# Kernel optimization log

Hardware: AMD Instinct MI355X
Metric: run time of the kernel (lower is better)

## Reference

```python
import jax, jax.numpy as jnp
import numpy as np

TAU = 0.28
EPS = 1e-08

def _l2norm(x):
    # F.normalize(dim=1): x / max(||x||, 1e-12)
    n = jnp.sqrt(jnp.sum(x * x, axis=1, keepdims=True))
    return x / jnp.maximum(n, 1e-12)

def setup_inputs() -> dict:
    key = jax.random.key(0)
    k1, k2 = jax.random.split(key)
    N, D = 16384, 64
    return {
        "user_embed": jax.random.normal(k1, (N, D), dtype=jnp.float32),
        "pos_item_embed": jax.random.normal(k2, (N, D), dtype=jnp.float32),
    }

def reference(user_embed, pos_item_embed):
    u = _l2norm(user_embed)          # [N, D]
    i = _l2norm(pos_item_embed)      # [N, D]
    pos_score = jnp.exp(jnp.sum(u * i, axis=-1) / TAU)          # [N]
    ui = jnp.matmul(u, i.T)          # [N, N]
    uu = jnp.matmul(u, u.T)          # [N, N]
    total = jnp.sum(jnp.exp((ui + uu) / TAU), axis=1)           # [N]
    na_loss = -jnp.log(pos_score / (total + EPS))
    return jnp.mean(na_loss)
```

## Files before the change

kernel.cpp:

```cpp
#include <hip/hip_runtime.h>
#include <hip/hip_bf16.h>

#define NROWS 16384
#define DIM 64
#define BCOLS 512
#define BROWS 1024
#define NCS (NROWS / BCOLS)
#define NRG (NROWS / BROWS)

static constexpr float TAU = 0.28f;
static constexpr float EPS = 1e-8f;
static constexpr float EXP2_SCALE = (float)(1.0 / (0.28 * 0.6931471805599453));
static constexpr float LN2F = 0.69314718055994530942f;

using short8 = __attribute__((ext_vector_type(8))) short;
using f32x4  = __attribute__((ext_vector_type(4))) float;

typedef __attribute__((address_space(1))) const unsigned char ga_t;
typedef __attribute__((address_space(3))) unsigned char la_t;

__global__ __launch_bounds__(256) void prep_kernel(
    const float* __restrict__ u, const float* __restrict__ v,
    __hip_bfloat16* __restrict__ a_out, __hip_bfloat16* __restrict__ w_out,
    float* __restrict__ p_out, float* __restrict__ total, float* __restrict__ out)
{
    const int lane = threadIdx.x & 63;
    const int wv   = threadIdx.x >> 6;
    const int row  = blockIdx.x * 4 + wv;

    const float uu = u[row * DIM + lane];
    const float ii = v[row * DIM + lane];
    float su = uu * uu, si = ii * ii, sd = uu * ii;
#pragma unroll
    for (int m = 1; m < 64; m <<= 1) {
        su += __shfl_xor(su, m, 64);
        si += __shfl_xor(si, m, 64);
        sd += __shfl_xor(sd, m, 64);
    }
    const float inv_u = 1.0f / fmaxf(sqrtf(su), 1e-12f);
    const float inv_i = 1.0f / fmaxf(sqrtf(si), 1e-12f);
    const float un = uu * inv_u;
    const float in = ii * inv_i;
    a_out[row * DIM + lane] = __float2bfloat16(EXP2_SCALE * un);
    w_out[row * DIM + lane] = __float2bfloat16(un + in);
    if (lane == 0) {
        p_out[row] = sd * inv_u * inv_i * (1.0f / TAU);
        total[row] = 0.0f;
    }
    if (blockIdx.x == 0 && threadIdx.x == 0) out[0] = 0.0f;
}

__global__ __launch_bounds__(512, 4) void score_kernel(
    const __hip_bfloat16* __restrict__ A, const __hip_bfloat16* __restrict__ W,
    float* __restrict__ total)
{
    __shared__ alignas(16) ushort blds[BCOLS * DIM];

    const int tid  = threadIdx.x;
    const int lane = tid & 63;
    const int wv   = tid >> 6;
    const int l15  = lane & 15;
    const int quad = lane >> 4;
    const int cs   = blockIdx.x & (NCS - 1);
    const int rg   = blockIdx.x >> 5;
    const int col0    = cs * BCOLS;
    const int rowbase = rg * BROWS;

    const ushort* Au = (const ushort*)A;
    const ushort* Wu = (const ushort*)W;

#pragma unroll
    for (int q = 0; q < 8; q++) {
        const int p = q * 512 + tid;
        const int j = p >> 3;
        const int c = (p & 7) ^ (j & 7);
        const ushort* g = Wu + (size_t)(col0 + j) * DIM + c * 8;
        __builtin_amdgcn_global_load_lds((ga_t*)g, (la_t*)&blds[(size_t)p * 8], 16, 0, 0);
    }
    __syncthreads();

    for (int si = 0; si < 4; si++) {
        const int r0 = rowbase + wv * 128 + si * 32;

        short8 af[2][2];
#pragma unroll
        for (int rs = 0; rs < 2; rs++)
#pragma unroll
            for (int kk = 0; kk < 2; kk++)
                af[rs][kk] = *(const short8*)(
                    Au + (size_t)(r0 + rs * 16 + l15) * DIM + kk * 32 + quad * 8);

        float rowsum[2][4];
#pragma unroll
        for (int rs = 0; rs < 2; rs++)
#pragma unroll
            for (int r = 0; r < 4; r++) rowsum[rs][r] = 0.0f;

#pragma unroll 8
        for (int ct = 0; ct < BCOLS / 16; ct++) {
            const int jl = ct * 16 + l15;
            const int sw = l15 & 7;
            const short8 b0 = *(const short8*)&blds[(size_t)(jl * 8 + (quad ^ sw)) * 8];
            const short8 b1 = *(const short8*)&blds[(size_t)(jl * 8 + ((4 + quad) ^ sw)) * 8];
#pragma unroll
            for (int rs = 0; rs < 2; rs++) {
                f32x4 acc = {0.f, 0.f, 0.f, 0.f};
                acc = __builtin_amdgcn_mfma_f32_16x16x32_bf16(af[rs][0], b0, acc, 0, 0, 0);
                acc = __builtin_amdgcn_mfma_f32_16x16x32_bf16(af[rs][1], b1, acc, 0, 0, 0);
#pragma unroll
                for (int r = 0; r < 4; r++)
                    rowsum[rs][r] += __builtin_amdgcn_exp2f(acc[r]);
            }
        }

#pragma unroll
        for (int m = 1; m < 16; m <<= 1)
#pragma unroll
            for (int rs = 0; rs < 2; rs++)
#pragma unroll
                for (int r = 0; r < 4; r++)
                    rowsum[rs][r] += __shfl_xor(rowsum[rs][r], m, 64);

        if (l15 == 0) {
#pragma unroll
            for (int rs = 0; rs < 2; rs++)
#pragma unroll
                for (int r = 0; r < 4; r++)
                    atomicAdd(&total[r0 + rs * 16 + quad * 4 + r], rowsum[rs][r]);
        }
    }
}

__global__ __launch_bounds__(256) void finalize_kernel(
    const float* __restrict__ total, const float* __restrict__ p,
    float* __restrict__ out)
{
    __shared__ float red[4];
    const int idx = blockIdx.x * 256 + threadIdx.x;
    float s = __log2f(total[idx] + EPS) * LN2F - p[idx];
#pragma unroll
    for (int m = 1; m < 64; m <<= 1) s += __shfl_xor(s, m, 64);
    if ((threadIdx.x & 63) == 0) red[threadIdx.x >> 6] = s;
    __syncthreads();
    if (threadIdx.x == 0)
        atomicAdd(out, (red[0] + red[1] + red[2] + red[3]) * (1.0f / (float)NROWS));
}

extern "C" void kernel_launch(void* const* d_in, const int* in_sizes, int n_in,
                              void* d_out, int out_size, void* d_ws, size_t ws_size,
                              hipStream_t stream) {
    const float* u = (const float*)d_in[0];
    const float* v = (const float*)d_in[1];

    char* ws = (char*)d_ws;
    __hip_bfloat16* a = (__hip_bfloat16*)(ws);
    __hip_bfloat16* w = (__hip_bfloat16*)(ws + (size_t)NROWS * DIM * 2);
    float* p   = (float*)(ws + (size_t)NROWS * DIM * 4);
    float* tot = (float*)(ws + (size_t)NROWS * DIM * 4 + (size_t)NROWS * 4);

    prep_kernel<<<NROWS / 4, 256, 0, stream>>>(u, v, a, w, p, tot, (float*)d_out);
    score_kernel<<<NRG * NCS, 512, 0, stream>>>(a, w, tot);
    finalize_kernel<<<NROWS / 256, 256, 0, stream>>>(tot, p, (float*)d_out);
}
```

Baseline: 103.9 us.

## Shrink score tiles to 256x256 and fuse finalize via last-block ticket

```diff
diff --git a/kernel.cpp b/kernel.cpp
--- a/kernel.cpp
+++ b/kernel.cpp
@@ -3,10 +3,11 @@
 
 #define NROWS 16384
 #define DIM 64
-#define BCOLS 512
-#define BROWS 1024
+#define BCOLS 256
+#define BROWS 256
 #define NCS (NROWS / BCOLS)
 #define NRG (NROWS / BROWS)
+#define NBLK (NCS * NRG)
 
 static constexpr float TAU = 0.28f;
 static constexpr float EPS = 1e-8f;
@@ -22,7 +23,7 @@
 __global__ __launch_bounds__(256) void prep_kernel(
     const float* __restrict__ u, const float* __restrict__ v,
     __hip_bfloat16* __restrict__ a_out, __hip_bfloat16* __restrict__ w_out,
-    float* __restrict__ p_out, float* __restrict__ total, float* __restrict__ out)
+    float* __restrict__ p_out, float* __restrict__ total, int* __restrict__ ticket)
 {
     const int lane = threadIdx.x & 63;
     const int wv   = threadIdx.x >> 6;
@@ -47,12 +48,13 @@
         p_out[row] = sd * inv_u * inv_i * (1.0f / TAU);
         total[row] = 0.0f;
     }
-    if (blockIdx.x == 0 && threadIdx.x == 0) out[0] = 0.0f;
+    if (blockIdx.x == 0 && threadIdx.x == 0) ticket[0] = 0;
 }
 
-__global__ __launch_bounds__(512, 4) void score_kernel(
+__global__ __launch_bounds__(256, 5) void score_kernel(
     const __hip_bfloat16* __restrict__ A, const __hip_bfloat16* __restrict__ W,
-    float* __restrict__ total)
+    float* __restrict__ total, const float* __restrict__ p,
+    int* __restrict__ ticket, float* __restrict__ out)
 {
     __shared__ alignas(16) ushort blds[BCOLS * DIM];
 
@@ -62,7 +64,7 @@
     const int l15  = lane & 15;
     const int quad = lane >> 4;
     const int cs   = blockIdx.x & (NCS - 1);
-    const int rg   = blockIdx.x >> 5;
+    const int rg   = blockIdx.x >> 6;
     const int col0    = cs * BCOLS;
     const int rowbase = rg * BROWS;
 
@@ -71,79 +73,86 @@
 
 #pragma unroll
     for (int q = 0; q < 8; q++) {
-        const int p = q * 512 + tid;
-        const int j = p >> 3;
-        const int c = (p & 7) ^ (j & 7);
+        const int pp = q * 256 + tid;
+        const int j  = pp >> 3;
+        const int c  = (pp & 7) ^ (j & 7);
         const ushort* g = Wu + (size_t)(col0 + j) * DIM + c * 8;
-        __builtin_amdgcn_global_load_lds((ga_t*)g, (la_t*)&blds[(size_t)p * 8], 16, 0, 0);
+        __builtin_amdgcn_global_load_lds((ga_t*)g, (la_t*)&blds[(size_t)pp * 8], 16, 0, 0);
+    }
+
+    const int r0 = rowbase + wv * 64;
+    short8 af[4][2];
+#pragma unroll
+    for (int rs = 0; rs < 4; rs++)
+#pragma unroll
+        for (int kk = 0; kk < 2; kk++)
+            af[rs][kk] = *(const short8*)(
+                Au + (size_t)(r0 + rs * 16 + l15) * DIM + kk * 32 + quad * 8);
+
+    float rowsum[4][4];
+#pragma unroll
+    for (int rs = 0; rs < 4; rs++)
+#pragma unroll
+        for (int r = 0; r < 4; r++) rowsum[rs][r] = 0.0f;
+
+    __syncthreads();
+
+#pragma unroll 4
+    for (int ct = 0; ct < BCOLS / 16; ct++) {
+        const int jl = ct * 16 + l15;
+        const int sw = l15 & 7;
+        const short8 b0 = *(const short8*)&blds[(size_t)(jl * 8 + (quad ^ sw)) * 8];
+        const short8 b1 = *(const short8*)&blds[(size_t)(jl * 8 + ((4 + quad) ^ sw)) * 8];
+#pragma unroll
+        for (int rs = 0; rs < 4; rs++) {
+            f32x4 acc = {0.f, 0.f, 0.f, 0.f};
+            acc = __builtin_amdgcn_mfma_f32_16x16x32_bf16(af[rs][0], b0, acc, 0, 0, 0);
+            acc = __builtin_amdgcn_mfma_f32_16x16x32_bf16(af[rs][1], b1, acc, 0, 0, 0);
+#pragma unroll
+            for (int r = 0; r < 4; r++)
+                rowsum[rs][r] += __builtin_amdgcn_exp2f(acc[r]);
+        }
+    }
+
+#pragma unroll
+    for (int m = 1; m < 16; m <<= 1)
+#pragma unroll
+        for (int rs = 0; rs < 4; rs++)
+#pragma unroll
+            for (int r = 0; r < 4; r++)
+                rowsum[rs][r] += __shfl_xor(rowsum[rs][r], m, 64);
+
+    if (l15 == 0) {
+#pragma unroll
+        for (int rs = 0; rs < 4; rs++)
+#pragma unroll
+            for (int r = 0; r < 4; r++)
+                atomicAdd(&total[r0 + rs * 16 + quad * 4 + r], rowsum[rs][r]);
+    }
+
+    __shared__ int lastflag;
+    __syncthreads();
+    if (tid == 0) {
+        __threadfence();
+        lastflag = (atomicAdd(ticket, 1) == NBLK - 1);
     }
     __syncthreads();
-
-    for (int si = 0; si < 4; si++) {
-        const int r0 = rowbase + wv * 128 + si * 32;
-
-        short8 af[2][2];
+    if (lastflag) {
+        __threadfence();
+        __shared__ float red[4];
+        float s = 0.0f;
 #pragma unroll
-        for (int rs = 0; rs < 2; rs++)
+        for (int k = 0; k < NROWS / 256; k++) {
+            const int idx = k * 256 + tid;
+            s += __log2f(total[idx] + EPS) * LN2F - p[idx];
+        }
 #pragma unroll
-            for (int kk = 0; kk < 2; kk++)
-                af[rs][kk] = *(const short8*)(
-                    Au + (size_t)(r0 + rs * 16 + l15) * DIM + kk * 32 + quad * 8);
-
-        float rowsum[2][4];
-#pragma unroll
-        for (int rs = 0; rs < 2; rs++)
-#pragma unroll
-            for (int r = 0; r < 4; r++) rowsum[rs][r] = 0.0f;
-
-#pragma unroll 8
-        for (int ct = 0; ct < BCOLS / 16; ct++) {
-            const int jl = ct * 16 + l15;
-            const int sw = l15 & 7;
-            const short8 b0 = *(const short8*)&blds[(size_t)(jl * 8 + (quad ^ sw)) * 8];
-            const short8 b1 = *(const short8*)&blds[(size_t)(jl * 8 + ((4 + quad) ^ sw)) * 8];
-#pragma unroll
-            for (int rs = 0; rs < 2; rs++) {
-                f32x4 acc = {0.f, 0.f, 0.f, 0.f};
-                acc = __builtin_amdgcn_mfma_f32_16x16x32_bf16(af[rs][0], b0, acc, 0, 0, 0);
-                acc = __builtin_amdgcn_mfma_f32_16x16x32_bf16(af[rs][1], b1, acc, 0, 0, 0);
-#pragma unroll
-                for (int r = 0; r < 4; r++)
-                    rowsum[rs][r] += __builtin_amdgcn_exp2f(acc[r]);
-            }
-        }
-
-#pragma unroll
-        for (int m = 1; m < 16; m <<= 1)
-#pragma unroll
-            for (int rs = 0; rs < 2; rs++)
-#pragma unroll
-                for (int r = 0; r < 4; r++)
-                    rowsum[rs][r] += __shfl_xor(rowsum[rs][r], m, 64);
-
-        if (l15 == 0) {
-#pragma unroll
-            for (int rs = 0; rs < 2; rs++)
-#pragma unroll
-                for (int r = 0; r < 4; r++)
-                    atomicAdd(&total[r0 + rs * 16 + quad * 4 + r], rowsum[rs][r]);
-        }
+        for (int m = 1; m < 64; m <<= 1) s += __shfl_xor(s, m, 64);
+        if ((tid & 63) == 0) red[tid >> 6] = s;
+        __syncthreads();
+        if (tid == 0)
+            out[0] = (red[0] + red[1] + red[2] + red[3]) * (1.0f / (float)NROWS);
     }
-}
-
-__global__ __launch_bounds__(256) void finalize_kernel(
-    const float* __restrict__ total, const float* __restrict__ p,
-    float* __restrict__ out)
-{
-    __shared__ float red[4];
-    const int idx = blockIdx.x * 256 + threadIdx.x;
-    float s = __log2f(total[idx] + EPS) * LN2F - p[idx];
-#pragma unroll
-    for (int m = 1; m < 64; m <<= 1) s += __shfl_xor(s, m, 64);
-    if ((threadIdx.x & 63) == 0) red[threadIdx.x >> 6] = s;
-    __syncthreads();
-    if (threadIdx.x == 0)
-        atomicAdd(out, (red[0] + red[1] + red[2] + red[3]) * (1.0f / (float)NROWS));
 }
 
 extern "C" void kernel_launch(void* const* d_in, const int* in_sizes, int n_in,
@@ -155,10 +164,10 @@
     char* ws = (char*)d_ws;
     __hip_bfloat16* a = (__hip_bfloat16*)(ws);
     __hip_bfloat16* w = (__hip_bfloat16*)(ws + (size_t)NROWS * DIM * 2);
-    float* p   = (float*)(ws + (size_t)NROWS * DIM * 4);
-    float* tot = (float*)(ws + (size_t)NROWS * DIM * 4 + (size_t)NROWS * 4);
+    float* p    = (float*)(ws + (size_t)NROWS * DIM * 4);
+    float* tot  = (float*)(ws + (size_t)NROWS * DIM * 4 + (size_t)NROWS * 4);
+    int*   tick = (int*)  (ws + (size_t)NROWS * DIM * 4 + (size_t)NROWS * 8);
 
-    prep_kernel<<<NROWS / 4, 256, 0, stream>>>(u, v, a, w, p, tot, (float*)d_out);
-    score_kernel<<<NRG * NCS, 512, 0, stream>>>(a, w, tot);
-    finalize_kernel<<<NROWS / 256, 256, 0, stream>>>(tot, p, (float*)d_out);
+    prep_kernel<<<NROWS / 4, 256, 0, stream>>>(u, v, a, w, p, tot, tick);
+    score_kernel<<<NBLK, 256, 0, stream>>>(a, w, tot, p, tick, (float*)d_out);
 }
```

Measured after the change: 173.9 us. 1.67x slower.
